# Kernel optimization log

Measured on AMD Instinct MI355X. Metric: run time of the kernel, lower is better.

The kernel has to match this reference:

```python
import jax, jax.numpy as jnp
import numpy as np

SIGMA = 1.0


def _sq_dists(a, b):
    # ||a_i - b_j||^2 via gemm: (n_a, n_b)
    aa = jnp.sum(a * a, axis=1)[:, None]
    bb = jnp.sum(b * b, axis=1)[None, :]
    ab = a @ b.T
    return jnp.maximum(aa + bb - 2.0 * ab, 0.0)


def _rbf(a, b, sigma):
    return jnp.exp(-_sq_dists(a, b) / (2.0 * sigma * sigma))


def setup_inputs() -> dict:
    key = jax.random.key(0)
    kx, ky = jax.random.split(key)
    x = jax.random.normal(kx, (4096, 1024), dtype=jnp.float32)
    y = jax.random.normal(ky, (4096, 1024), dtype=jnp.float32)
    return {"x": x, "y": y}


def reference(x, y):
    # Flatten non-batch dims (module accepts (n, f1, f2, ...))
    xf = x.reshape(x.shape[0], -1)
    yf = y.reshape(y.shape[0], -1)
    n = xf.shape[0]
    m = yf.shape[0]

    k_xx = _rbf(xf, xf, SIGMA)
    k_yy = _rbf(yf, yf, SIGMA)
    k_xy = _rbf(xf, yf, SIGMA)

    # Unbiased estimator: exclude diagonal of k_xx / k_yy
    sum_xx = jnp.sum(k_xx) - jnp.trace(k_xx)
    sum_yy = jnp.sum(k_yy) - jnp.trace(k_yy)
    sum_xy = jnp.sum(k_xy)

    mmd2 = (sum_xx / (n * (n - 1))
            + sum_yy / (m * (m - 1))
            - 2.0 * sum_xy / (n * m))
    return mmd2
```

## Files before the change

kernel.cpp:

```cpp
#include <hip/hip_runtime.h>


#define NROWS 4096
#define KDIM  1024
#define BM 128
#define BN 128
#define SLAB 128
#define SLABBYTES (BM * SLAB)
#define NT   32
#define TRI  528
#define NXY  1024

typedef unsigned short u16;
typedef unsigned char  u8;
typedef __attribute__((ext_vector_type(8))) int   int8v;
typedef __attribute__((ext_vector_type(4))) int   int4v;
typedef __attribute__((ext_vector_type(8))) short short8;
typedef __attribute__((ext_vector_type(4))) float f32x4;

__global__ void mmd_zero_sums(float* sums) {
    if (threadIdx.x < 3) sums[threadIdx.x] = 0.0f;
}

__device__ __forceinline__ void async_copy16(const void* g, void* l) {
    __builtin_amdgcn_global_load_lds(
        (const __attribute__((address_space(1))) unsigned int*)g,
        (__attribute__((address_space(3))) unsigned int*)l, 16, 0, 0);
}

__global__ __launch_bounds__(256) void mmd_prep8(const float* __restrict__ x,
                                                 const float* __restrict__ y,
                                                 float* __restrict__ aa,
                                                 float* __restrict__ bb,
                                                 u8* __restrict__ xb,
                                                 u8* __restrict__ yb,
                                                 float* __restrict__ sums) {
    if (blockIdx.x == 0 && blockIdx.y == 0 && threadIdx.x < 3) sums[threadIdx.x] = 0.0f;
    const int row = blockIdx.x;
    const float* src = blockIdx.y ? y : x;
    float* ndst = blockIdx.y ? bb : aa;
    u8* bdst    = blockIdx.y ? yb : xb;
    const float4 v = ((const float4*)(src + (size_t)row * KDIM))[threadIdx.x];
    int p = 0;
    p = __builtin_amdgcn_cvt_pk_fp8_f32(v.x, v.y, p, false);
    p = __builtin_amdgcn_cvt_pk_fp8_f32(v.z, v.w, p, true);
    ((int*)(bdst + (size_t)row * KDIM))[threadIdx.x] = p;
    float s = v.x * v.x + v.y * v.y + v.z * v.z + v.w * v.w;
    #pragma unroll
    for (int off = 32; off; off >>= 1) s += __shfl_down(s, off, 64);
    __shared__ float ws[4];
    if ((threadIdx.x & 63) == 0) ws[threadIdx.x >> 6] = s;
    __syncthreads();
    if (threadIdx.x == 0) ndst[row] = ws[0] + ws[1] + ws[2] + ws[3];
}

__global__ __launch_bounds__(256, 2) void mmd_tile_fp8(const u8* __restrict__ xb,
                                                       const u8* __restrict__ yb,
                                                       const float* __restrict__ aa,
                                                       const float* __restrict__ bb,
                                                       float* __restrict__ sums) {
    int mode, ti, tj;
    const int bid = blockIdx.x;
    if (bid < NXY) {
        mode = 2;
        const int st = bid >> 6;
        const int wi = bid & 63;
        ti = (st >> 2) * 8 + (wi >> 3);
        tj = (st & 3) * 8 + (wi & 7);
    } else {
        int s = bid - NXY;
        mode = (s >= TRI) ? 1 : 0;
        if (s >= TRI) s -= TRI;
        int t = (int)(32.5f - sqrtf(32.5f * 32.5f - 2.0f * (float)s));
        while (t > 0 && t * (65 - t) / 2 > s) t--;
        while ((t + 1) * (64 - t) / 2 <= s) t++;
        ti = t;
        tj = t + (s - t * (65 - t) / 2);
    }

    const u8*    __restrict__ A  = (mode == 1) ? yb : xb;
    const u8*    __restrict__ B  = (mode == 0) ? xb : yb;
    const float* __restrict__ na = (mode == 1) ? bb : aa;
    const float* __restrict__ nb = (mode == 0) ? aa : bb;

    __shared__ u8 As[2 * SLABBYTES];
    __shared__ u8 Bs[2 * SLABBYTES];

    const int t = threadIdx.x;
    const int w = t >> 6;
    const int l = t & 63;

    const int lrow = l >> 3;
    const int gch  = (l & 7) ^ lrow;
    const u8* aS[4]; const u8* bS[4]; int ldso[4];
    #pragma unroll
    for (int a = 0; a < 4; a++) {
        const int blk = a * 4 + w;
        const int row = blk * 8 + lrow;
        aS[a] = A + (size_t)(ti * BM + row) * KDIM + gch * 16;
        bS[a] = B + (size_t)(tj * BN + row) * KDIM + gch * 16;
        ldso[a] = blk * 1024 + l * 16;
    }
#define STAGE(buf, kk) do { \
        _Pragma("unroll") \
        for (int a = 0; a < 4; a++) { \
            async_copy16(aS[a] + (kk), &As[(buf) * SLABBYTES + ldso[a]]); \
            async_copy16(bS[a] + (kk), &Bs[(buf) * SLABBYTES + ldso[a]]); \
        } \
    } while (0)

    const int wm = (w >> 1) * 64;
    const int wn = (w & 1) * 64;
    const int r  = l & 15;
    const int h  = l >> 4;
    const int s0 = (2 * h) ^ (r & 7);
    const int aB0 = (wm + r) * 128 + s0 * 16;
    const int bB0 = (wn + r) * 128 + s0 * 16;

    f32x4 acc[4][4] = {};

    STAGE(0, 0);
    int cur = 0;
    for (int k0 = 0; k0 < KDIM; k0 += SLAB) {
        __syncthreads();
        if (k0 + SLAB < KDIM) STAGE(cur ^ 1, k0 + SLAB);

        const u8* Ab = &As[cur * SLABBYTES];
        const u8* Bb = &Bs[cur * SLABBYTES];
        int8v af[4], bf[4];
        #pragma unroll
        for (int im = 0; im < 4; im++) {
            union { int8v v; int4v hh[2]; } u;
            u.hh[0] = *(const int4v*)(Ab + (aB0 + im * 2048));
            u.hh[1] = *(const int4v*)(Ab + ((aB0 + im * 2048) ^ 16));
            af[im] = u.v;
        }
        #pragma unroll
        for (int in = 0; in < 4; in++) {
            union { int8v v; int4v hh[2]; } u;
            u.hh[0] = *(const int4v*)(Bb + (bB0 + in * 2048));
            u.hh[1] = *(const int4v*)(Bb + ((bB0 + in * 2048) ^ 16));
            bf[in] = u.v;
        }
        #pragma unroll
        for (int im = 0; im < 4; im++)
            #pragma unroll
            for (int in = 0; in < 4; in++)
                acc[im][in] = __builtin_amdgcn_mfma_scale_f32_16x16x128_f8f6f4(
                    af[im], bf[in], acc[im][in],
                    0 , 0 ,
                    0, 127,
                    0, 127);
        cur ^= 1;
    }
#undef STAGE

    const int giBase = ti * BM + wm + h * 4;
    const int gjBase = tj * BN + wn + r;
    float nav[4][4], nbv[4];
    #pragma unroll
    for (int im = 0; im < 4; im++)
        #pragma unroll
        for (int rr = 0; rr < 4; rr++) nav[im][rr] = na[giBase + im * 16 + rr];
    #pragma unroll
    for (int in = 0; in < 4; in++) nbv[in] = nb[gjBase + in * 16];

    float lsum = 0.0f;
    #pragma unroll
    for (int im = 0; im < 4; im++) {
        #pragma unroll
        for (int in = 0; in < 4; in++) {
            const int gj = gjBase + in * 16;
            #pragma unroll
            for (int rr = 0; rr < 4; rr++) {
                const int gi = giBase + im * 16 + rr;
                float d = fmaxf(nav[im][rr] + nbv[in] - 2.0f * acc[im][in][rr], 0.0f);
                float v = __expf(-0.5f * d);
                float wgt = (mode == 2) ? 1.0f : ((gj > gi) ? 2.0f : 0.0f);
                lsum = fmaf(wgt, v, lsum);
            }
        }
    }
    #pragma unroll
    for (int off = 32; off; off >>= 1) lsum += __shfl_down(lsum, off, 64);
    __shared__ float red[4];
    if (l == 0) red[w] = lsum;
    __syncthreads();
    if (t == 0) atomicAdd(&sums[mode], red[0] + red[1] + red[2] + red[3]);
}

__device__ __forceinline__ unsigned pk_bf16(float lo, float hi) {
    unsigned ul = __float_as_uint(lo); ul += 0x7fffu + ((ul >> 16) & 1u);
    unsigned uh = __float_as_uint(hi); uh += 0x7fffu + ((uh >> 16) & 1u);
    return (ul >> 16) | (uh & 0xffff0000u);
}

__global__ __launch_bounds__(256) void mmd_row_norms(const float* __restrict__ x,
                                                     const float* __restrict__ y,
                                                     float* __restrict__ aa,
                                                     float* __restrict__ bb) {
    const int row = blockIdx.x;
    const float* src = blockIdx.y ? y : x;
    float* dst = blockIdx.y ? bb : aa;
    const float4 v = ((const float4*)(src + (size_t)row * KDIM))[threadIdx.x];
    float s = v.x * v.x + v.y * v.y + v.z * v.z + v.w * v.w;
    #pragma unroll
    for (int off = 32; off; off >>= 1) s += __shfl_down(s, off, 64);
    __shared__ float ws[4];
    if ((threadIdx.x & 63) == 0) ws[threadIdx.x >> 6] = s;
    __syncthreads();
    if (threadIdx.x == 0) dst[row] = ws[0] + ws[1] + ws[2] + ws[3];
}

#define LDST 40
#define BK 32
__global__ __launch_bounds__(256) void mmd_tile_v2(const float* __restrict__ x,
                                                   const float* __restrict__ y,
                                                   const float* __restrict__ aa,
                                                   const float* __restrict__ bb,
                                                   float* __restrict__ sums) {
    const int mode = blockIdx.z;
    const int ti = blockIdx.y, tj = blockIdx.x;
    if (mode < 2 && tj < ti) return;
    const float* __restrict__ A  = (mode == 1) ? y : x;
    const float* __restrict__ B  = (mode == 0) ? x : y;
    const float* __restrict__ na = (mode == 1) ? bb : aa;
    const float* __restrict__ nb = (mode == 0) ? aa : bb;
    __shared__ u16 As[BM * LDST];
    __shared__ u16 Bs[BN * LDST];
    const int t = threadIdx.x;
    const int srow = t >> 1;
    const int skb  = (t & 1) * 16;
    const float* aptr = A + (size_t)(ti * BM + srow) * KDIM + skb;
    const float* bptr = B + (size_t)(tj * BN + srow) * KDIM + skb;
    u16* aDst = &As[srow * LDST + skb];
    u16* bDst = &Bs[srow * LDST + skb];
    const int l  = t & 63;
    const int wv = t >> 6;
    const int wm = (wv >> 1) * 64;
    const int wn = (wv & 1) * 64;
    const int q  = l >> 4;
    const int c  = l & 15;
    const u16* aFrag = &As[(wm + c) * LDST + q * 8];
    const u16* bFrag = &Bs[(wn + c) * LDST + q * 8];
    f32x4 acc[4][4] = {};
    float4 pa[4], pb[4];
    #pragma unroll
    for (int i = 0; i < 4; i++) {
        pa[i] = *(const float4*)(aptr + i * 4);
        pb[i] = *(const float4*)(bptr + i * 4);
    }
    for (int k0 = 0; k0 < KDIM; k0 += BK) {
        uint4 w0, w1;
        w0.x = pk_bf16(pa[0].x, pa[0].y); w0.y = pk_bf16(pa[0].z, pa[0].w);
        w0.z = pk_bf16(pa[1].x, pa[1].y); w0.w = pk_bf16(pa[1].z, pa[1].w);
        w1.x = pk_bf16(pa[2].x, pa[2].y); w1.y = pk_bf16(pa[2].z, pa[2].w);
        w1.z = pk_bf16(pa[3].x, pa[3].y); w1.w = pk_bf16(pa[3].z, pa[3].w);
        __syncthreads();
        ((uint4*)aDst)[0] = w0; ((uint4*)aDst)[1] = w1;
        w0.x = pk_bf16(pb[0].x, pb[0].y); w0.y = pk_bf16(pb[0].z, pb[0].w);
        w0.z = pk_bf16(pb[1].x, pb[1].y); w0.w = pk_bf16(pb[1].z, pb[1].w);
        w1.x = pk_bf16(pb[2].x, pb[2].y); w1.y = pk_bf16(pb[2].z, pb[2].w);
        w1.z = pk_bf16(pb[3].x, pb[3].y); w1.w = pk_bf16(pb[3].z, pb[3].w);
        ((uint4*)bDst)[0] = w0; ((uint4*)bDst)[1] = w1;
        __syncthreads();
        if (k0 + BK < KDIM) {
            #pragma unroll
            for (int i = 0; i < 4; i++) {
                pa[i] = *(const float4*)(aptr + k0 + BK + i * 4);
                pb[i] = *(const float4*)(bptr + k0 + BK + i * 4);
            }
        }
        short8 af[4], bf[4];
        #pragma unroll
        for (int im = 0; im < 4; im++) af[im] = *(const short8*)(aFrag + im * 16 * LDST);
        #pragma unroll
        for (int in = 0; in < 4; in++) bf[in] = *(const short8*)(bFrag + in * 16 * LDST);
        #pragma unroll
        for (int im = 0; im < 4; im++)
            #pragma unroll
            for (int in = 0; in < 4; in++)
                acc[im][in] = __builtin_amdgcn_mfma_f32_16x16x32_bf16(af[im], bf[in], acc[im][in], 0, 0, 0);
    }
    const int giBase = ti * BM + wm + q * 4;
    const int gjBase = tj * BN + wn + c;
    float lsum = 0.0f;
    #pragma unroll
    for (int im = 0; im < 4; im++) {
        #pragma unroll
        for (int in = 0; in < 4; in++) {
            const int gj = gjBase + in * 16;
            #pragma unroll
            for (int rr = 0; rr < 4; rr++) {
                const int gi = giBase + im * 16 + rr;
                float d = fmaxf(na[gi] + nb[gj] - 2.0f * acc[im][in][rr], 0.0f);
                float v = __expf(-0.5f * d);
                float wgt = (mode == 2) ? 1.0f : ((gj > gi) ? 2.0f : 0.0f);
                lsum = fmaf(wgt, v, lsum);
            }
        }
    }
    #pragma unroll
    for (int off = 32; off; off >>= 1) lsum += __shfl_down(lsum, off, 64);
    __shared__ float red[4];
    if (l == 0) red[wv] = lsum;
    __syncthreads();
    if (t == 0) atomicAdd(&sums[mode], red[0] + red[1] + red[2] + red[3]);
}

__global__ void mmd_finalize(const float* __restrict__ sums, float* __restrict__ out, int n, int m) {
    if (threadIdx.x == 0) {
        float fn = (float)n, fm = (float)m;
        out[0] = sums[0] / (fn * (fn - 1.0f))
               + sums[1] / (fm * (fm - 1.0f))
               - 2.0f * sums[2] / (fn * fm);
    }
}

extern "C" void kernel_launch(void* const* d_in, const int* in_sizes, int n_in,
                              void* d_out, int out_size, void* d_ws, size_t ws_size,
                              hipStream_t stream) {
    const float* x = (const float*)d_in[0];
    const float* y = (const float*)d_in[1];
    float* out = (float*)d_out;

    char* ws = (char*)d_ws;
    float* aa   = (float*)(ws);
    float* bb   = (float*)(ws + 16384);
    float* sums = (float*)(ws + 32768);
    u8*    xb   = (u8*)(ws + 33024);
    u8*    yb   = xb + (size_t)NROWS * KDIM;

    const size_t needed = 33024 + 2 * (size_t)NROWS * KDIM;
    const int n = in_sizes[0] / KDIM;
    const int m = in_sizes[1] / KDIM;

    if (ws_size >= needed) {
        hipLaunchKernelGGL(mmd_prep8, dim3(NROWS, 2), dim3(256), 0, stream,
                           x, y, aa, bb, xb, yb, sums);
        hipLaunchKernelGGL(mmd_tile_fp8, dim3(NXY + 2 * TRI), dim3(256), 0, stream,
                           xb, yb, aa, bb, sums);
    } else {
        hipLaunchKernelGGL(mmd_zero_sums, dim3(1), dim3(64), 0, stream, sums);
        hipLaunchKernelGGL(mmd_row_norms, dim3(NROWS, 2), dim3(256), 0, stream, x, y, aa, bb);
        hipLaunchKernelGGL(mmd_tile_v2, dim3(NROWS / BN, NROWS / BM, 3), dim3(256), 0, stream,
                           x, y, aa, bb, sums);
    }
    hipLaunchKernelGGL(mmd_finalize, dim3(1), dim3(1), 0, stream, sums, out, n, m);
}
```

Measured before the change: 132.0 us.

## Drop LDS double buffering to single buffer and raise occupancy to three blocks

Replaces the double-buffered async LDS staging with a single buffer per operand, so each K slab is loaded and then synchronised before compute. Launch bounds go from 2 to 3 blocks per CU to use the freed LDS for more resident blocks. The aim is to hide latency through more concurrent blocks instead of intra-block prefetch. In exchange it adds a barrier per slab and removes the overlap of global loads with MFMA within a block.

```diff
diff --git a/kernel.cpp b/kernel.cpp
--- a/kernel.cpp
+++ b/kernel.cpp
@@ -54,7 +54,7 @@
     if (threadIdx.x == 0) ndst[row] = ws[0] + ws[1] + ws[2] + ws[3];
 }
 
-__global__ __launch_bounds__(256, 2) void mmd_tile_fp8(const u8* __restrict__ xb,
+__global__ __launch_bounds__(256, 3) void mmd_tile_fp8(const u8* __restrict__ xb,
                                                        const u8* __restrict__ yb,
                                                        const float* __restrict__ aa,
                                                        const float* __restrict__ bb,
@@ -83,8 +83,8 @@
     const float* __restrict__ na = (mode == 1) ? bb : aa;
     const float* __restrict__ nb = (mode == 0) ? aa : bb;
 
-    __shared__ u8 As[2 * SLABBYTES];
-    __shared__ u8 Bs[2 * SLABBYTES];
+    __shared__ u8 As[SLABBYTES];
+    __shared__ u8 Bs[SLABBYTES];
 
     const int t = threadIdx.x;
     const int w = t >> 6;
@@ -101,13 +101,6 @@
         bS[a] = B + (size_t)(tj * BN + row) * KDIM + gch * 16;
         ldso[a] = blk * 1024 + l * 16;
     }
-#define STAGE(buf, kk) do { \
-        _Pragma("unroll") \
-        for (int a = 0; a < 4; a++) { \
-            async_copy16(aS[a] + (kk), &As[(buf) * SLABBYTES + ldso[a]]); \
-            async_copy16(bS[a] + (kk), &Bs[(buf) * SLABBYTES + ldso[a]]); \
-        } \
-    } while (0)
 
     const int wm = (w >> 1) * 64;
     const int wn = (w & 1) * 64;
@@ -119,27 +112,28 @@
 
     f32x4 acc[4][4] = {};
 
-    STAGE(0, 0);
-    int cur = 0;
     for (int k0 = 0; k0 < KDIM; k0 += SLAB) {
+        if (k0) __syncthreads();
+        #pragma unroll
+        for (int a = 0; a < 4; a++) {
+            async_copy16(aS[a] + k0, &As[ldso[a]]);
+            async_copy16(bS[a] + k0, &Bs[ldso[a]]);
+        }
         __syncthreads();
-        if (k0 + SLAB < KDIM) STAGE(cur ^ 1, k0 + SLAB);
-
-        const u8* Ab = &As[cur * SLABBYTES];
-        const u8* Bb = &Bs[cur * SLABBYTES];
+
         int8v af[4], bf[4];
         #pragma unroll
         for (int im = 0; im < 4; im++) {
             union { int8v v; int4v hh[2]; } u;
-            u.hh[0] = *(const int4v*)(Ab + (aB0 + im * 2048));
-            u.hh[1] = *(const int4v*)(Ab + ((aB0 + im * 2048) ^ 16));
+            u.hh[0] = *(const int4v*)(As + (aB0 + im * 2048));
+            u.hh[1] = *(const int4v*)(As + ((aB0 + im * 2048) ^ 16));
             af[im] = u.v;
         }
         #pragma unroll
         for (int in = 0; in < 4; in++) {
             union { int8v v; int4v hh[2]; } u;
-            u.hh[0] = *(const int4v*)(Bb + (bB0 + in * 2048));
-            u.hh[1] = *(const int4v*)(Bb + ((bB0 + in * 2048) ^ 16));
+            u.hh[0] = *(const int4v*)(Bs + (bB0 + in * 2048));
+            u.hh[1] = *(const int4v*)(Bs + ((bB0 + in * 2048) ^ 16));
             bf[in] = u.v;
         }
         #pragma unroll
@@ -151,9 +145,7 @@
                     0 , 0 ,
                     0, 127,
                     0, 127);
-        cur ^= 1;
-    }
-#undef STAGE
+    }
 
     const int giBase = ti * BM + wm + h * 4;
     const int gjBase = tj * BN + wn + r;
```

Result: faster. 125.8 us (-4.7%).

## Switch to 32x32x64 FP8 MFMA with smaller K slabs and fuse finalize

Applied to the files above, without the earlier changes.

The FP8 tile kernel now uses 32x32x64 scaled MFMA instructions with a 2x2 accumulator grid per wave instead of 4x4 of 16x16x128. The K slab is halved to 64 bytes, and the LDS swizzle and load layout are reworked to match. Launch bounds now request 4 blocks per SU, which shrinks LDS per block and allows more occupancy. The finalize kernel launch is removed by having the last block, counted through an atomic counter, compute the output. This trades one kernel launch for fence and atomic overhead, and it doubles the number of K-loop barriers.

```diff
diff --git a/kernel.cpp b/kernel.cpp
--- a/kernel.cpp
+++ b/kernel.cpp
@@ -5,18 +5,20 @@
 #define KDIM  1024
 #define BM 128
 #define BN 128
-#define SLAB 128
-#define SLABBYTES (BM * SLAB)
+#define SLAB 64
+#define SLABB (BM * SLAB)
 #define NT   32
 #define TRI  528
 #define NXY  1024
+#define NBLK (NXY + 2 * TRI)
 
 typedef unsigned short u16;
 typedef unsigned char  u8;
-typedef __attribute__((ext_vector_type(8))) int   int8v;
-typedef __attribute__((ext_vector_type(4))) int   int4v;
-typedef __attribute__((ext_vector_type(8))) short short8;
-typedef __attribute__((ext_vector_type(4))) float f32x4;
+typedef __attribute__((ext_vector_type(8)))  int   int8v;
+typedef __attribute__((ext_vector_type(4)))  int   int4v;
+typedef __attribute__((ext_vector_type(16))) float f32x16;
+typedef __attribute__((ext_vector_type(8)))  short short8;
+typedef __attribute__((ext_vector_type(4)))  float f32x4;
 
 __global__ void mmd_zero_sums(float* sums) {
     if (threadIdx.x < 3) sums[threadIdx.x] = 0.0f;
@@ -34,8 +36,12 @@
                                                  float* __restrict__ bb,
                                                  u8* __restrict__ xb,
                                                  u8* __restrict__ yb,
-                                                 float* __restrict__ sums) {
-    if (blockIdx.x == 0 && blockIdx.y == 0 && threadIdx.x < 3) sums[threadIdx.x] = 0.0f;
+                                                 float* __restrict__ sums,
+                                                 unsigned* __restrict__ cnt) {
+    if (blockIdx.x == 0 && blockIdx.y == 0) {
+        if (threadIdx.x < 3) sums[threadIdx.x] = 0.0f;
+        if (threadIdx.x == 3) *cnt = 0u;
+    }
     const int row = blockIdx.x;
     const float* src = blockIdx.y ? y : x;
     float* ndst = blockIdx.y ? bb : aa;
@@ -54,11 +60,13 @@
     if (threadIdx.x == 0) ndst[row] = ws[0] + ws[1] + ws[2] + ws[3];
 }
 
-__global__ __launch_bounds__(256, 2) void mmd_tile_fp8(const u8* __restrict__ xb,
+__global__ __launch_bounds__(256, 4) void mmd_tile_fp8(const u8* __restrict__ xb,
                                                        const u8* __restrict__ yb,
                                                        const float* __restrict__ aa,
                                                        const float* __restrict__ bb,
-                                                       float* __restrict__ sums) {
+                                                       float* __restrict__ sums,
+                                                       unsigned* __restrict__ cnt,
+                                                       float* __restrict__ out) {
     int mode, ti, tj;
     const int bid = blockIdx.x;
     if (bid < NXY) {
@@ -83,41 +91,42 @@
     const float* __restrict__ na = (mode == 1) ? bb : aa;
     const float* __restrict__ nb = (mode == 0) ? aa : bb;
 
-    __shared__ u8 As[2 * SLABBYTES];
-    __shared__ u8 Bs[2 * SLABBYTES];
+    __shared__ u8 As[2 * SLABB];
+    __shared__ u8 Bs[2 * SLABB];
 
     const int t = threadIdx.x;
     const int w = t >> 6;
     const int l = t & 63;
 
-    const int lrow = l >> 3;
-    const int gch  = (l & 7) ^ lrow;
-    const u8* aS[4]; const u8* bS[4]; int ldso[4];
-    #pragma unroll
-    for (int a = 0; a < 4; a++) {
-        const int blk = a * 4 + w;
-        const int row = blk * 8 + lrow;
+    const int lrow = l >> 2;
+    const int gch  = (l & 3) ^ ((l >> 3) & 3);
+    const u8* aS[2]; const u8* bS[2]; int ldso[2];
+    #pragma unroll
+    for (int a = 0; a < 2; a++) {
+        const int row = a * 64 + w * 16 + lrow;
         aS[a] = A + (size_t)(ti * BM + row) * KDIM + gch * 16;
         bS[a] = B + (size_t)(tj * BN + row) * KDIM + gch * 16;
-        ldso[a] = blk * 1024 + l * 16;
+        ldso[a] = (a * 64 + w * 16) * 64 + l * 16;
     }
 #define STAGE(buf, kk) do { \
         _Pragma("unroll") \
-        for (int a = 0; a < 4; a++) { \
-            async_copy16(aS[a] + (kk), &As[(buf) * SLABBYTES + ldso[a]]); \
-            async_copy16(bS[a] + (kk), &Bs[(buf) * SLABBYTES + ldso[a]]); \
+        for (int a = 0; a < 2; a++) { \
+            async_copy16(aS[a] + (kk), &As[(buf) * SLABB + ldso[a]]); \
+            async_copy16(bS[a] + (kk), &Bs[(buf) * SLABB + ldso[a]]); \
         } \
     } while (0)
 
-    const int wm = (w >> 1) * 64;
-    const int wn = (w & 1) * 64;
-    const int r  = l & 15;
-    const int h  = l >> 4;
-    const int s0 = (2 * h) ^ (r & 7);
-    const int aB0 = (wm + r) * 128 + s0 * 16;
-    const int bB0 = (wn + r) * 128 + s0 * 16;
-
-    f32x4 acc[4][4] = {};
+    const int wm  = (w >> 1) * 64;
+    const int wn  = (w & 1) * 64;
+    const int m32 = l & 31;
+    const int h2  = l >> 5;
+    const int sw  = (l >> 1) & 3;
+    const int c0s = ((2 * h2) ^ sw) * 16;
+    const int c1s = ((2 * h2 + 1) ^ sw) * 16;
+    const int aB0 = (wm + m32) * 64;
+    const int bB0 = (wn + m32) * 64;
+
+    f32x16 acc[2][2] = {};
 
     STAGE(0, 0);
     int cur = 0;
@@ -125,28 +134,28 @@
         __syncthreads();
         if (k0 + SLAB < KDIM) STAGE(cur ^ 1, k0 + SLAB);
 
-        const u8* Ab = &As[cur * SLABBYTES];
-        const u8* Bb = &Bs[cur * SLABBYTES];
-        int8v af[4], bf[4];
-        #pragma unroll
-        for (int im = 0; im < 4; im++) {
+        const u8* Ab = &As[cur * SLABB];
+        const u8* Bb = &Bs[cur * SLABB];
+        int8v af[2], bf[2];
+        #pragma unroll
+        for (int im = 0; im < 2; im++) {
             union { int8v v; int4v hh[2]; } u;
-            u.hh[0] = *(const int4v*)(Ab + (aB0 + im * 2048));
-            u.hh[1] = *(const int4v*)(Ab + ((aB0 + im * 2048) ^ 16));
+            u.hh[0] = *(const int4v*)(Ab + aB0 + im * 2048 + c0s);
+            u.hh[1] = *(const int4v*)(Ab + aB0 + im * 2048 + c1s);
             af[im] = u.v;
         }
         #pragma unroll
-        for (int in = 0; in < 4; in++) {
+        for (int in = 0; in < 2; in++) {
             union { int8v v; int4v hh[2]; } u;
-            u.hh[0] = *(const int4v*)(Bb + (bB0 + in * 2048));
-            u.hh[1] = *(const int4v*)(Bb + ((bB0 + in * 2048) ^ 16));
+            u.hh[0] = *(const int4v*)(Bb + bB0 + in * 2048 + c0s);
+            u.hh[1] = *(const int4v*)(Bb + bB0 + in * 2048 + c1s);
             bf[in] = u.v;
         }
         #pragma unroll
-        for (int im = 0; im < 4; im++)
-            #pragma unroll
-            for (int in = 0; in < 4; in++)
-                acc[im][in] = __builtin_amdgcn_mfma_scale_f32_16x16x128_f8f6f4(
+        for (int im = 0; im < 2; im++)
+            #pragma unroll
+            for (int in = 0; in < 2; in++)
+                acc[im][in] = __builtin_amdgcn_mfma_scale_f32_32x32x64_f8f6f4(
                     af[im], bf[in], acc[im][in],
                     0 , 0 ,
                     0, 127,
@@ -155,26 +164,18 @@
     }
 #undef STAGE
 
-    const int giBase = ti * BM + wm + h * 4;
-    const int gjBase = tj * BN + wn + r;
-    float nav[4][4], nbv[4];
-    #pragma unroll
-    for (int im = 0; im < 4; im++)
-        #pragma unroll
-        for (int rr = 0; rr < 4; rr++) nav[im][rr] = na[giBase + im * 16 + rr];
-    #pragma unroll
-    for (int in = 0; in < 4; in++) nbv[in] = nb[gjBase + in * 16];
-
     float lsum = 0.0f;
     #pragma unroll
-    for (int im = 0; im < 4; im++) {
-        #pragma unroll
-        for (int in = 0; in < 4; in++) {
-            const int gj = gjBase + in * 16;
-            #pragma unroll
-            for (int rr = 0; rr < 4; rr++) {
-                const int gi = giBase + im * 16 + rr;
-                float d = fmaxf(nav[im][rr] + nbv[in] - 2.0f * acc[im][in][rr], 0.0f);
+    for (int in = 0; in < 2; in++) {
+        const int gj = tj * BN + wn + in * 32 + m32;
+        const float nbv = nb[gj];
+        #pragma unroll
+        for (int im = 0; im < 2; im++) {
+            const int giB = ti * BM + wm + im * 32 + 4 * h2;
+            #pragma unroll
+            for (int r16 = 0; r16 < 16; r16++) {
+                const int gi = giB + (r16 & 3) + 8 * (r16 >> 2);
+                float d = fmaxf(na[gi] + nbv - 2.0f * acc[im][in][r16], 0.0f);
                 float v = __expf(-0.5f * d);
                 float wgt = (mode == 2) ? 1.0f : ((gj > gi) ? 2.0f : 0.0f);
                 lsum = fmaf(wgt, v, lsum);
@@ -186,7 +187,21 @@
     __shared__ float red[4];
     if (l == 0) red[w] = lsum;
     __syncthreads();
-    if (t == 0) atomicAdd(&sums[mode], red[0] + red[1] + red[2] + red[3]);
+    if (t == 0) {
+        atomicAdd(&sums[mode], red[0] + red[1] + red[2] + red[3]);
+        __threadfence();
+        const unsigned old = atomicAdd(cnt, 1u);
+        if (old == NBLK - 1) {
+            __threadfence();
+            const float sxx = ((volatile float*)sums)[0];
+            const float syy = ((volatile float*)sums)[1];
+            const float sxy = ((volatile float*)sums)[2];
+            const float fn = (float)NROWS, fm = (float)NROWS;
+            out[0] = sxx / (fn * (fn - 1.0f))
+                   + syy / (fm * (fm - 1.0f))
+                   - 2.0f * sxy / (fn * fm);
+        }
+    }
 }
 
 __device__ __forceinline__ unsigned pk_bf16(float lo, float hi) {
@@ -325,11 +340,12 @@
     float* out = (float*)d_out;
 
     char* ws = (char*)d_ws;
-    float* aa   = (float*)(ws);
-    float* bb   = (float*)(ws + 16384);
-    float* sums = (float*)(ws + 32768);
-    u8*    xb   = (u8*)(ws + 33024);
-    u8*    yb   = xb + (size_t)NROWS * KDIM;
+    float*    aa   = (float*)(ws);
+    float*    bb   = (float*)(ws + 16384);
+    float*    sums = (float*)(ws + 32768);
+    unsigned* cnt  = (unsigned*)(ws + 32780);
+    u8*       xb   = (u8*)(ws + 33024);
+    u8*       yb   = xb + (size_t)NROWS * KDIM;
 
     const size_t needed = 33024 + 2 * (size_t)NROWS * KDIM;
     const int n = in_sizes[0] / KDIM;
@@ -337,14 +353,14 @@
 
     if (ws_size >= needed) {
         hipLaunchKernelGGL(mmd_prep8, dim3(NROWS, 2), dim3(256), 0, stream,
-                           x, y, aa, bb, xb, yb, sums);
-        hipLaunchKernelGGL(mmd_tile_fp8, dim3(NXY + 2 * TRI), dim3(256), 0, stream,
-                           xb, yb, aa, bb, sums);
+                           x, y, aa, bb, xb, yb, sums, cnt);
+        hipLaunchKernelGGL(mmd_tile_fp8, dim3(NBLK), dim3(256), 0, stream,
+                           xb, yb, aa, bb, sums, cnt, out);
     } else {
         hipLaunchKernelGGL(mmd_zero_sums, dim3(1), dim3(64), 0, stream, sums);
         hipLaunchKernelGGL(mmd_row_norms, dim3(NROWS, 2), dim3(256), 0, stream, x, y, aa, bb);
         hipLaunchKernelGGL(mmd_tile_v2, dim3(NROWS / BN, NROWS / BM, 3), dim3(256), 0, stream,
                            x, y, aa, bb, sums);
-    }
-    hipLaunchKernelGGL(mmd_finalize, dim3(1), dim3(1), 0, stream, sums, out, n, m);
-}
+        hipLaunchKernelGGL(mmd_finalize, dim3(1), dim3(1), 0, stream, sums, out, n, m);
+    }
+}
```

New measurement: 193.6 us. 46.7% more time.
